# Performance work log

Hardware: AMD Instinct MI355X
Metric: run time of the kernel (lower is better)

The kernel has to match this reference:

```python
import jax, jax.numpy as jnp
import numpy as np

NH, DH, DHR = 16, 128, 64  # heads, head dim, decoupled rope dim
ROPE_BASE = 10000.0

def _rope(x):
    # x: (B, L, H, Dr) with Dr even; interleaved-pair RoPE (torchtune style)
    B, L, H, Dr = x.shape
    pos = jnp.arange(L, dtype=jnp.float32)
    inv_freq = 1.0 / (ROPE_BASE ** (jnp.arange(0, Dr, 2, dtype=jnp.float32) / Dr))
    ang = pos[:, None] * inv_freq[None, :]          # (L, Dr/2)
    cos = jnp.cos(ang)[None, :, None, :].astype(x.dtype)
    sin = jnp.sin(ang)[None, :, None, :].astype(x.dtype)
    x1, x2 = x[..., 0::2], x[..., 1::2]
    out = jnp.stack([x1 * cos - x2 * sin, x1 * sin + x2 * cos], axis=-1)
    return out.reshape(B, L, H, Dr)

def setup_inputs() -> dict:
    key = jax.random.key(0)
    ks = jax.random.split(key, 9)
    s = 0.02
    return {
        'x':     jax.random.normal(ks[0], (2, 2048, 2048), jnp.float32),
        'W_DKV': jax.random.normal(ks[1], (2048, 682), jnp.float32) * s,
        'W_UK':  jax.random.normal(ks[2], (682, 2048), jnp.float32) * s,
        'W_UV':  jax.random.normal(ks[3], (682, 2048), jnp.float32) * s,
        'W_KR':  jax.random.normal(ks[4], (2048, 64), jnp.float32) * s,
        'W_DQ':  jax.random.normal(ks[5], (2048, 682), jnp.float32) * s,
        'W_UQ':  jax.random.normal(ks[6], (682, 2048), jnp.float32) * s,
        'W_QR':  jax.random.normal(ks[7], (682, 1024), jnp.float32) * s,
        'W_O':   jax.random.normal(ks[8], (2048, 2048), jnp.float32) * s,
    }

def reference(x, W_DKV, W_UK, W_UV, W_KR, W_DQ, W_UQ, W_QR, W_O):
    B, L, D = x.shape
    # --- KV path ---
    c_KV = x @ W_DKV                                   # (B, L, dc)
    k_C = (c_KV @ W_UK).reshape(B, L, NH, DH)          # content keys
    k_R = _rope((x @ W_KR).reshape(B, L, 1, DHR))      # shared rope key head
    k_R = jnp.broadcast_to(k_R, (B, L, NH, DHR))
    k = jnp.concatenate([k_C, k_R], axis=-1)           # (B, L, NH, DH+DHR)
    v = (c_KV @ W_UV).reshape(B, L, NH, DH)
    # --- Q path ---
    c_Q = x @ W_DQ                                     # (B, L, dc')
    q_C = (c_Q @ W_UQ).reshape(B, L, NH, DH)
    q_R = _rope((c_Q @ W_QR).reshape(B, L, NH, DHR))
    q = jnp.concatenate([q_C, q_R], axis=-1)           # (B, L, NH, DH+DHR)
    # --- attention (causal) ---
    scale = 1.0 / jnp.sqrt(jnp.float32(DH + DHR))
    scores = jnp.einsum('blhd,bmhd->bhlm', q, k) * scale
    causal = jnp.tril(jnp.ones((L, L), dtype=bool))
    scores = jnp.where(causal[None, None], scores, jnp.finfo(scores.dtype).min)
    attn = jax.nn.softmax(scores, axis=-1)
    o = jnp.einsum('bhlm,bmhd->blhd', attn, v).reshape(B, L, NH * DH)
    return o @ W_O
```

## Files before the change

### kernel.cpp

```cpp
#include <hip/hip_runtime.h>
#include <stdint.h>

typedef __attribute__((ext_vector_type(8))) __bf16 bf16x8;
typedef __attribute__((ext_vector_type(4))) float f32x4;

#define DEVI static __device__ __forceinline__

DEVI uint16_t f2b(float f) {
  uint32_t u = __float_as_uint(f);
  u += 0x7FFFu + ((u >> 16) & 1u);
  return (uint16_t)(u >> 16);
}
DEVI float b2f(uint16_t b) { return __uint_as_float(((uint32_t)b) << 16); }

DEVI void gl_lds16(const void* g, void* l) {
  __builtin_amdgcn_global_load_lds((const __attribute__((address_space(1))) void*)g,
                                   (__attribute__((address_space(3))) void*)l, 16, 0, 0);
}

DEVI f32x4 mfma16(bf16x8 a, bf16x8 b, f32x4 c) {
  return __builtin_amdgcn_mfma_f32_16x16x32_bf16(a, b, c, 0, 0, 0);
}

#define BARX asm volatile("s_barrier" ::: "memory")
#define WLG0 asm volatile("s_waitcnt lgkmcnt(0)" ::: "memory")
#define WV4 asm volatile("s_waitcnt vmcnt(4)" ::: "memory")
#define PRIO1 __builtin_amdgcn_s_setprio(1)
#define PRIO0 __builtin_amdgcn_s_setprio(0)

static constexpr size_t OFF_XB = 0;
static constexpr size_t OFF_WD = 8388608;
static constexpr size_t OFF_WUKV = OFF_WD + 3670016;
static constexpr size_t OFF_WUQR = OFF_WUKV + 3145728;
static constexpr size_t OFF_WO = OFF_WUQR + 2359296;
static constexpr size_t OFF_CD = OFF_WO + 4194304;
static constexpr size_t OFF_CUKV = OFF_CD + 7340032;
static constexpr size_t OFF_CUQR = OFF_CUKV + 16777216;
static constexpr size_t OFF_VT = OFF_CUQR + 12582912;

__global__ void pre_kernel(const float* __restrict__ x, const float* __restrict__ Wdkv,
                           const float* __restrict__ Wuk, const float* __restrict__ Wuv,
                           const float* __restrict__ Wkr, const float* __restrict__ Wdq,
                           const float* __restrict__ Wuq, const float* __restrict__ Wqr,
                           const float* __restrict__ Wo, uint16_t* __restrict__ ws) {
  const int bid = blockIdx.x;
  const int t = threadIdx.x;
  if (bid >= 3264) {
    int id = (bid - 3264) * 256 + t;
    float4 v = ((const float4*)x)[id];
    uint16_t o[4] = {f2b(v.x), f2b(v.y), f2b(v.z), f2b(v.w)};
    *(uint64_t*)&ws[OFF_XB + (size_t)id * 4] = *(uint64_t*)o;
    return;
  }
  const float* W;
  uint16_t* Wt;
  int Kw, Nw, Kp, nx, rb;
  if (bid < 384) {
    W = Wdkv; Wt = ws + OFF_WD; Kw = 2048; Nw = 682; Kp = 2048; nx = 12; rb = bid;
  } else if (bid < 768) {
    W = Wdq; Wt = ws + OFF_WD + (size_t)768 * 2048; Kw = 2048; Nw = 682; Kp = 2048; nx = 12; rb = bid - 384;
  } else if (bid < 896) {
    W = Wkr; Wt = ws + OFF_WD + (size_t)1536 * 2048; Kw = 2048; Nw = 64; Kp = 2048; nx = 4; rb = bid - 768;
  } else if (bid < 1280) {
    W = Wuk; Wt = ws + OFF_WUKV; Kw = 682; Nw = 2048; Kp = 768; nx = 32; rb = bid - 896;
  } else if (bid < 1664) {
    W = Wuv; Wt = ws + OFF_WUKV + (size_t)2048 * 768; Kw = 682; Nw = 2048; Kp = 768; nx = 32; rb = bid - 1280;
  } else if (bid < 2048) {
    W = Wuq; Wt = ws + OFF_WUQR; Kw = 682; Nw = 2048; Kp = 768; nx = 32; rb = bid - 1664;
  } else if (bid < 2240) {
    W = Wqr; Wt = ws + OFF_WUQR + (size_t)2048 * 768; Kw = 682; Nw = 1024; Kp = 768; nx = 16; rb = bid - 2048;
  } else {
    W = Wo; Wt = ws + OFF_WO; Kw = 2048; Nw = 2048; Kp = 2048; nx = 32; rb = bid - 2240;
  }
  const int n0 = (rb % nx) * 64, k0 = (rb / nx) * 64;
  __shared__ uint16_t T[64][72];
#pragma unroll
  for (int p = 0; p < 2; ++p) {
    int r = p * 32 + (t >> 3);
    int c0 = (t & 7) * 8;
    int gr = k0 + r;
#pragma unroll
    for (int e = 0; e < 8; ++e) {
      int gc = n0 + c0 + e;
      float v = (gr < Kw && gc < Nw) ? W[(size_t)gr * Nw + gc] : 0.f;
      T[c0 + e][r] = f2b(v);
    }
  }
  __syncthreads();
#pragma unroll
  for (int p = 0; p < 2; ++p) {
    int dr = p * 32 + (t >> 3);
    int mc = (t & 7) * 8;
    uint16_t tmp[8];
#pragma unroll
    for (int e = 0; e < 8; ++e) tmp[e] = T[dr][mc + e];
    *(uint64_t*)&Wt[(size_t)(n0 + dr) * Kp + k0 + mc] = ((uint64_t*)tmp)[0];
    *(uint64_t*)&Wt[(size_t)(n0 + dr) * Kp + k0 + mc + 4] = ((uint64_t*)tmp)[1];
  }
}

template <int BM, bool F32OUT>
__global__ __launch_bounds__(512, 2) void gemm8(const uint16_t* __restrict__ A, int lda,
                                                const uint16_t* __restrict__ Bt,
                                                void* __restrict__ Cv, int ldc, int K) {
  constexpr int MF = BM / 32;
  constexpr int MH = MF / 2;
  constexpr int AL = BM / 128;
  constexpr int ABYTES = BM * 128;
  __shared__ char lds[2 * BM * 128 + 2 * 256 * 128];
  char* const LB = lds + 2 * ABYTES;
  const int tid = threadIdx.x;
  const int lane = tid & 63;
  const int lr = lane & 15, lgb = (lane >> 4) * 16;
  const int wid = tid >> 6;
  const int g = wid >> 2;
  const int wc = (wid & 3) * 64;
  const int rA0 = g * (BM / 2) + lr;
  const int rB0 = wc + lr;
  const size_t row0 = (size_t)blockIdx.y * BM, col0 = (size_t)blockIdx.x * 256;
  const char* Agb = (const char*)(A + row0 * lda);
  const char* Btb = (const char*)(Bt + col0 * K);
  const size_t ldab = (size_t)lda * 2;
  const size_t ldbb = (size_t)K * 2;
  const int nk = K >> 6;
  const int ni = nk >> 1;

  f32x4 acc[MF][4] = {};
  bf16x8 aF[MH][2], bF[4][2];

  auto stageA = [&](int kt, int buf, int hf) {
#pragma unroll
    for (int j = 0; j < AL; ++j) {
      int c = j * 512 + tid;
      int cl = c ^ (((c >> 5) & 1) << 1);
      int row = hf * (BM / 2) + (cl >> 3);
      gl_lds16(Agb + (size_t)row * ldab + (size_t)kt * 128 + (cl & 7) * 16,
               lds + buf * ABYTES + hf * (ABYTES / 2) + (j * 512 + (tid & 0x1C0)) * 16);
    }
  };
  auto stageB = [&](int kt, int buf, int hf) {
#pragma unroll
    for (int j = 0; j < 2; ++j) {
      int c = j * 512 + tid;
      int cl = c ^ (((c >> 5) & 1) << 1);
      int row = hf * 128 + (cl >> 3);
      gl_lds16(Btb + (size_t)row * ldbb + (size_t)kt * 128 + (cl & 7) * 16,
               LB + buf * 32768 + hf * 16384 + (j * 512 + (tid & 0x1C0)) * 16);
    }
  };
  auto ldAm = [&](int buf, int mb) {
#pragma unroll
    for (int m = 0; m < MH; ++m) {
      int r = rA0 + (mb + m) * 16;
      int ro = r * 128;
      int sw = ((r >> 2) & 1) << 5;
#pragma unroll
      for (int kk = 0; kk < 2; ++kk)
        aF[m][kk] = *(const bf16x8*)(lds + buf * ABYTES + ((ro + kk * 64 + lgb) ^ sw));
    }
  };
  auto ldBn = [&](int buf, int nb) {
#pragma unroll
    for (int n = 0; n < 2; ++n) {
      int r = rB0 + (nb + n) * 16;
      int ro = r * 128;
      int sw = ((r >> 2) & 1) << 5;
#pragma unroll
      for (int kk = 0; kk < 2; ++kk)
        bF[nb + n][kk] = *(const bf16x8*)(LB + buf * 32768 + ((ro + kk * 64 + lgb) ^ sw));
    }
  };
  auto mmac = [&](int mb, int nb) {
#pragma unroll
    for (int m = 0; m < MH; ++m)
#pragma unroll
      for (int n = 0; n < 2; ++n)
#pragma unroll
        for (int kk = 0; kk < 2; ++kk)
          acc[mb + m][nb + n] = mfma16(aF[m][kk], bF[nb + n][kk], acc[mb + m][nb + n]);
  };

  stageA(0, 0, 0); stageA(0, 0, 1); stageB(0, 0, 0); stageB(0, 0, 1);
  stageB(1, 1, 0); stageB(1, 1, 1);
  WV4; BARX;

  for (int i = 0; i < ni; ++i) {
    const int t1 = 2 * i + 1;
    const int tn = (2 * i + 2 < nk) ? 2 * i + 2 : nk - 1;
    const int tn1 = (2 * i + 3 < nk) ? 2 * i + 3 : nk - 1;
    ldAm(0, 0); ldBn(0, 0); stageA(t1, 1, 0);
    BARX; WLG0; PRIO1; mmac(0, 0); PRIO0; BARX;
    ldBn(0, 2); stageA(t1, 1, 1);
    BARX; WLG0; PRIO1; mmac(0, 2); PRIO0; BARX;
    ldAm(0, MH); stageB(tn, 0, 0);
    BARX; WLG0; PRIO1; mmac(MH, 0); PRIO0; BARX;
    stageB(tn, 0, 1);
    BARX; PRIO1; mmac(MH, 2); PRIO0; WV4; BARX;
    ldAm(1, 0); ldBn(1, 0); stageA(tn, 0, 0);
    BARX; WLG0; PRIO1; mmac(0, 0); PRIO0; BARX;
    ldBn(1, 2); stageA(tn, 0, 1);
    BARX; WLG0; PRIO1; mmac(0, 2); PRIO0; BARX;
    ldAm(1, MH); stageB(tn1, 1, 0);
    BARX; WLG0; PRIO1; mmac(MH, 0); PRIO0; BARX;
    stageB(tn1, 1, 1);
    BARX; PRIO1; mmac(MH, 2); PRIO0; WV4; BARX;
  }
  asm volatile("s_waitcnt vmcnt(0)" ::: "memory");

#pragma unroll
  for (int m = 0; m < MF; ++m)
#pragma unroll
    for (int n = 0; n < 4; ++n)
#pragma unroll
      for (int j = 0; j < 4; ++j) {
        size_t row = row0 + g * (BM / 2) + m * 16 + (lane >> 4) * 4 + j;
        size_t col = col0 + wc + n * 16 + lr;
        if (F32OUT)
          ((float*)Cv)[row * ldc + col] = acc[m][n][j];
        else
          ((uint16_t*)Cv)[row * ldc + col] = f2b(acc[m][n][j]);
      }
}

__global__ void misc_kernel(uint16_t* __restrict__ cd, uint16_t* __restrict__ cuqr,
                            const uint16_t* __restrict__ cukv, uint16_t* __restrict__ vt) {
  const int bid = blockIdx.x;
  const int t = threadIdx.x;
  if (bid < 512) {
    int id = bid * 256 + t;
    int row = id >> 5, i = id & 31;
    int pos = row & 2047;
    float invf = exp2f(-13.287712379549449f * (float)i / 32.f);
    float ang = (float)pos * invf;
    float s, c;
    sincosf(ang, &s, &c);
    size_t base = (size_t)row * 1792 + 1536 + 2 * i;
    float x1 = b2f(cd[base]), x2 = b2f(cd[base + 1]);
    cd[base] = f2b(x1 * c - x2 * s);
    cd[base + 1] = f2b(x1 * s + x2 * c);
    return;
  }
  if (bid < 8704) {
    int id = (bid - 512) * 256 + t;
    int row = id >> 9;
    int rem = id & 511;
    int h = rem >> 5, i = rem & 31;
    int pos = row & 2047;
    float invf = exp2f(-13.287712379549449f * (float)i / 32.f);
    float ang = (float)pos * invf;
    float s, c;
    sincosf(ang, &s, &c);
    size_t base = (size_t)row * 3072 + 2048 + h * 64 + 2 * i;
    float x1 = b2f(cuqr[base]), x2 = b2f(cuqr[base + 1]);
    cuqr[base] = f2b(x1 * c - x2 * s);
    cuqr[base + 1] = f2b(x1 * s + x2 * c);
    return;
  }
  const int idx = bid - 8704;
  const int mt = idx & 31, dt = (idx >> 5) & 1, bh = idx >> 6;
  const int b = bh >> 4, h = bh & 15;
  const int m0 = mt * 64, d0 = dt * 64;
  __shared__ uint16_t T[64][72];
#pragma unroll
  for (int p = 0; p < 2; ++p) {
    int r = p * 32 + (t >> 3), c8 = (t & 7) * 8;
    const uint16_t* s = &cukv[((size_t)(b * 2048 + m0 + r)) * 4096 + 2048 + h * 128 + d0 + c8];
    uint16_t tmp[8];
    ((uint64_t*)tmp)[0] = ((const uint64_t*)s)[0];
    ((uint64_t*)tmp)[1] = ((const uint64_t*)s)[1];
#pragma unroll
    for (int e = 0; e < 8; ++e) T[c8 + e][r] = tmp[e];
  }
  __syncthreads();
#pragma unroll
  for (int p = 0; p < 2; ++p) {
    int dr = p * 32 + (t >> 3), mc = (t & 7) * 8;
    uint16_t tmp[8];
#pragma unroll
    for (int e = 0; e < 8; ++e) tmp[e] = T[dr][mc + e];
    uint16_t* dstp = &vt[((size_t)(bh * 128 + d0 + dr)) * 2048 + m0 + mc];
    ((uint64_t*)dstp)[0] = ((uint64_t*)tmp)[0];
    ((uint64_t*)dstp)[1] = ((uint64_t*)tmp)[1];
  }
}

__global__ __launch_bounds__(512, 2) void attn_kernel(const uint16_t* __restrict__ cuqr,
                                                      const uint16_t* __restrict__ cukv,
                                                      const uint16_t* __restrict__ cd,
                                                      const uint16_t* __restrict__ vt,
                                                      uint16_t* __restrict__ obuf) {
  __shared__ uint16_t Ks[2][64 * 192];
  __shared__ uint16_t Vs[2][128 * 64];
  __shared__ uint16_t Ps[8 * 16 * 64];
  const int tid = threadIdx.x;
  const int wid = tid >> 6, lane = tid & 63;
  const int lr = lane & 15, lg = lane >> 4;
  const int bid = blockIdx.x;
  const int wg = (bid & 7) * 32 + (bid >> 3);
  const int pairi = wg & 7;
  const int bh = wg >> 3;
  const int b = bh >> 4, h = bh & 15;
  const float sc2 = 0.07216878364870323f * 1.4426950408889634f;

  const char* Kcb = (const char*)cukv + (size_t)b * 2048 * 8192 + h * 256;
  const char* Krb = (const char*)cd + (size_t)b * 2048 * 3584 + 3072;
  const char* Vb = (const char*)vt + (size_t)bh * 524288;
  char* const Ks0 = (char*)Ks[0];
  char* const Vs0 = (char*)Vs[0];
  char* PwB = (char*)(Ps + wid * 1024);

  const char* kbase[3];
  size_t kstep[3];
  int klds[3];
#pragma unroll
  for (int i = 0; i < 3; ++i) {
    int c = i * 512 + tid;
    int r = c / 24, c16 = c % 24;
    klds[i] = r * 384 + ((c16 * 16) ^ ((r & 7) << 4));
    if (c16 < 16) {
      kbase[i] = Kcb + (size_t)r * 8192 + c16 * 16;
      kstep[i] = (size_t)64 * 8192;
    } else {
      kbase[i] = Krb + (size_t)r * 3584 + (c16 - 16) * 16;
      kstep[i] = (size_t)64 * 3584;
    }
  }
  const char* vbase[2];
  int vlds[2];
#pragma unroll
  for (int i = 0; i < 2; ++i) {
    int c = i * 512 + tid;
    int d = c >> 3, c16 = c & 7;
    vlds[i] = d * 128 + ((c16 * 16) ^ ((d & 7) << 4));
    vbase[i] = Vb + (size_t)d * 4096 + c16 * 16;
  }

  for (int ph = 0; ph < 2; ++ph) {
    const int qt = ph ? (15 - pairi) : pairi;
    const int q0 = qt * 128;
    const int nt = 2 * (qt + 1);
    const int qrow = q0 + wid * 16 + lr;
    bf16x8 qf[6];
    {
      const char* Qcp = (const char*)cuqr + (size_t)(b * 2048 + qrow) * 6144 + h * 256 + lg * 16;
      const char* Qrp =
          (const char*)cuqr + (size_t)(b * 2048 + qrow) * 6144 + 4096 + h * 128 + lg * 16;
#pragma unroll
      for (int kb = 0; kb < 4; ++kb) qf[kb] = *(const bf16x8*)(Qcp + kb * 64);
#pragma unroll
      for (int kb = 0; kb < 2; ++kb) qf[4 + kb] = *(const bf16x8*)(Qrp + kb * 64);
    }
    f32x4 o[8] = {};
    float mrun[4], lrun[4];
#pragma unroll
    for (int j = 0; j < 4; ++j) { mrun[j] = -INFINITY; lrun[j] = 0.f; }

    const char* kp[3];
    const char* vp[2];
    bf16x8 kreg[3], vreg[2];
#pragma unroll
    for (int i = 0; i < 3; ++i) kp[i] = kbase[i];
#pragma unroll
    for (int i = 0; i < 2; ++i) vp[i] = vbase[i];
#pragma unroll
    for (int i = 0; i < 3; ++i) { kreg[i] = *(const bf16x8*)kp[i]; kp[i] += kstep[i]; }
#pragma unroll
    for (int i = 0; i < 2; ++i) { vreg[i] = *(const bf16x8*)vp[i]; vp[i] += 128; }
#pragma unroll
    for (int i = 0; i < 3; ++i) *(bf16x8*)(Ks0 + klds[i]) = kreg[i];
#pragma unroll
    for (int i = 0; i < 2; ++i) *(bf16x8*)(Vs0 + vlds[i]) = vreg[i];
    __syncthreads();

    for (int t = 0; t < nt; ++t) {
      const bool more = (t + 1 < nt);
      if (more) {
#pragma unroll
        for (int i = 0; i < 3; ++i) { kreg[i] = *(const bf16x8*)kp[i]; kp[i] += kstep[i]; }
#pragma unroll
        for (int i = 0; i < 2; ++i) { vreg[i] = *(const bf16x8*)vp[i]; vp[i] += 128; }
      }
      const int cb = t & 1;
      const char* KsB = Ks0 + cb * 24576;
      const char* VsB = Vs0 + cb * 16384;
      if (t * 64 <= q0 + wid * 16 + 15) {
        f32x4 s[4] = {};
        __builtin_amdgcn_s_setprio(1);
#pragma unroll
        for (int n = 0; n < 4; ++n) {
          int r = n * 16 + lr;
          const char* kptr = KsB + r * 384;
          int sw = (r & 7) << 4;
#pragma unroll
          for (int kb = 0; kb < 6; ++kb)
            s[n] = mfma16(qf[kb], *(const bf16x8*)(kptr + ((kb * 64 + lg * 16) ^ sw)), s[n]);
        }
        __builtin_amdgcn_s_setprio(0);
        if (t * 64 + 63 > q0 + wid * 16) {
#pragma unroll
          for (int n = 0; n < 4; ++n)
#pragma unroll
            for (int j = 0; j < 4; ++j)
              if (t * 64 + n * 16 + lr > q0 + wid * 16 + lg * 4 + j) s[n][j] = -INFINITY;
        }
        float pm[4];
#pragma unroll
        for (int j = 0; j < 4; ++j) {
          float v = fmaxf(fmaxf(s[0][j], s[1][j]), fmaxf(s[2][j], s[3][j]));
          v = fmaxf(v, __shfl_xor(v, 1));
          v = fmaxf(v, __shfl_xor(v, 2));
          v = fmaxf(v, __shfl_xor(v, 4));
          v = fmaxf(v, __shfl_xor(v, 8));
          pm[j] = v;
        }
        bool exceed = false;
#pragma unroll
        for (int j = 0; j < 4; ++j) exceed |= (pm[j] > mrun[j] + 76.8f);
        if (__any(exceed)) {
          float alpha[4];
#pragma unroll
          for (int j = 0; j < 4; ++j) {
            float mn = fmaxf(mrun[j], pm[j]);
            alpha[j] = exp2f((mrun[j] - mn) * sc2);
            mrun[j] = mn;
            lrun[j] *= alpha[j];
          }
#pragma unroll
          for (int n2 = 0; n2 < 8; ++n2)
#pragma unroll
            for (int j = 0; j < 4; ++j) o[n2][j] *= alpha[j];
        }
        float rs[4] = {0.f, 0.f, 0.f, 0.f};
#pragma unroll
        for (int n = 0; n < 4; ++n)
#pragma unroll
          for (int j = 0; j < 4; ++j) {
            float p = exp2f((s[n][j] - mrun[j]) * sc2);
            rs[j] += p;
            int row = lg * 4 + j;
            *(uint16_t*)(PwB + row * 128 + ((((n * 16 + lr)) * 2) ^ ((row & 7) << 4))) = f2b(p);
          }
#pragma unroll
        for (int j = 0; j < 4; ++j) lrun[j] += rs[j];
        __builtin_amdgcn_s_setprio(1);
#pragma unroll
        for (int kb2 = 0; kb2 < 2; ++kb2) {
          bf16x8 pa = *(const bf16x8*)(PwB + lr * 128 + ((kb2 * 64 + lg * 16) ^ ((lr & 7) << 4)));
#pragma unroll
          for (int n2 = 0; n2 < 8; ++n2) {
            int vr = n2 * 16 + lr;
            o[n2] = mfma16(
                pa, *(const bf16x8*)(VsB + vr * 128 + ((kb2 * 64 + lg * 16) ^ ((vr & 7) << 4))),
                o[n2]);
          }
        }
        __builtin_amdgcn_s_setprio(0);
      }
      if (more) {
        char* KsN = Ks0 + (cb ^ 1) * 24576;
        char* VsN = Vs0 + (cb ^ 1) * 16384;
#pragma unroll
        for (int i = 0; i < 3; ++i) *(bf16x8*)(KsN + klds[i]) = kreg[i];
#pragma unroll
        for (int i = 0; i < 2; ++i) *(bf16x8*)(VsN + vlds[i]) = vreg[i];
      }
      __syncthreads();
    }
#pragma unroll
    for (int j = 0; j < 4; ++j) {
      float v = lrun[j];
      v += __shfl_xor(v, 1);
      v += __shfl_xor(v, 2);
      v += __shfl_xor(v, 4);
      v += __shfl_xor(v, 8);
      lrun[j] = v;
    }
    float inv[4];
#pragma unroll
    for (int j = 0; j < 4; ++j) inv[j] = 1.f / lrun[j];
#pragma unroll
    for (int n2 = 0; n2 < 8; ++n2)
#pragma unroll
      for (int j = 0; j < 4; ++j) {
        size_t row = (size_t)b * 2048 + q0 + wid * 16 + lg * 4 + j;
        size_t col = (size_t)h * 128 + n2 * 16 + lr;
        obuf[row * 2048 + col] = f2b(o[n2][j] * inv[j]);
      }
  }
}

extern "C" void kernel_launch(void* const* d_in, const int* in_sizes, int n_in,
                              void* d_out, int out_size, void* d_ws, size_t ws_size,
                              hipStream_t stream) {
  (void)in_sizes; (void)n_in; (void)out_size; (void)ws_size;
  const float* x = (const float*)d_in[0];
  const float* Wdkv = (const float*)d_in[1];
  const float* Wuk = (const float*)d_in[2];
  const float* Wuv = (const float*)d_in[3];
  const float* Wkr = (const float*)d_in[4];
  const float* Wdq = (const float*)d_in[5];
  const float* Wuq = (const float*)d_in[6];
  const float* Wqr = (const float*)d_in[7];
  const float* Wo = (const float*)d_in[8];
  uint16_t* ws = (uint16_t*)d_ws;

  uint16_t* xb = ws + OFF_XB;
  uint16_t* obuf = ws + OFF_XB;
  uint16_t* wd = ws + OFF_WD;
  uint16_t* wukv = ws + OFF_WUKV;
  uint16_t* wuqr = ws + OFF_WUQR;
  uint16_t* wo = ws + OFF_WO;
  uint16_t* cd = ws + OFF_CD;
  uint16_t* cukv = ws + OFF_CUKV;
  uint16_t* cuqr = ws + OFF_CUQR;
  uint16_t* vtb = ws + OFF_VT;

  pre_kernel<<<11456, 256, 0, stream>>>(x, Wdkv, Wuk, Wuv, Wkr, Wdq, Wuq, Wqr, Wo, ws);
  gemm8<128, false><<<dim3(7, 32), 512, 0, stream>>>(xb, 2048, wd, cd, 1792, 2048);
  gemm8<256, false><<<dim3(16, 16), 512, 0, stream>>>(cd, 1792, wukv, cukv, 4096, 768);
  gemm8<256, false><<<dim3(12, 16), 512, 0, stream>>>(cd + 768, 1792, wuqr, cuqr, 3072, 768);
  misc_kernel<<<10752, 256, 0, stream>>>(cd, cuqr, cukv, vtb);
  attn_kernel<<<256, 512, 0, stream>>>(cuqr, cukv, cd, vtb, obuf);
  gemm8<128, true><<<dim3(8, 32), 512, 0, stream>>>(obuf, 2048, wo, d_out, 2048, 2048);
}
```

Baseline: 265.3 us.

## Add pipelined 128x256 GEMM kernel for down-projection and output projection

Adds a new gemm4p kernel that double-buffers A and B tiles in LDS. Loads are staggered so global-to-LDS copies of the next k-tiles overlap with MFMA work on the current ones, with priority bumps around the MFMA phases. It replaces gemm8<128> for the x@W_D and o@W_O GEMMs to hide memory latency. The cost is higher LDS use (96KB per block) and tighter coupling of barriers to the K-tile count, which assumes nk is even.

```diff
diff --git a/kernel.cpp b/kernel.cpp
--- a/kernel.cpp
+++ b/kernel.cpp
@@ -222,6 +222,115 @@
       }
 }
 
+template <bool F32OUT>
+__global__ __launch_bounds__(512, 2) void gemm4p(const uint16_t* __restrict__ A, int lda,
+                                                 const uint16_t* __restrict__ Bt,
+                                                 void* __restrict__ Cv, int ldc, int K) {
+  constexpr int ABYTES = 128 * 128;
+  __shared__ char lds[2 * ABYTES + 2 * 32768];
+  char* const LB = lds + 2 * ABYTES;
+  const int tid = threadIdx.x;
+  const int lane = tid & 63;
+  const int lr = lane & 15, lgb = (lane >> 4) * 16;
+  const int wid = tid >> 6;
+  const int g = wid >> 2;
+  const int wc = (wid & 3) * 64;
+  const int rA0 = g * 64 + lr;
+  const int rB0 = wc + lr;
+  const size_t row0 = (size_t)blockIdx.y * 128, col0 = (size_t)blockIdx.x * 256;
+  const char* Agb = (const char*)(A + row0 * lda);
+  const char* Btb = (const char*)(Bt + col0 * K);
+  const size_t ldab = (size_t)lda * 2;
+  const size_t ldbb = (size_t)K * 2;
+  const int nk = K >> 6;
+  const int ni = nk >> 1;
+
+  f32x4 acc[4][4] = {};
+  bf16x8 aF[2][2], bF[4][2];
+
+  auto stageA = [&](int kt, int buf) {
+#pragma unroll
+    for (int j = 0; j < 2; ++j) {
+      int c = j * 512 + tid;
+      int cl = c ^ (((c >> 5) & 1) << 1);
+      gl_lds16(Agb + (size_t)(cl >> 3) * ldab + (size_t)kt * 128 + (cl & 7) * 16,
+               lds + buf * ABYTES + (j * 512 + (tid & 0x1C0)) * 16);
+    }
+  };
+  auto stageBfull = [&](int kt, int buf) {
+#pragma unroll
+    for (int j = 0; j < 4; ++j) {
+      int c = j * 512 + tid;
+      int cl = c ^ (((c >> 5) & 1) << 1);
+      gl_lds16(Btb + (size_t)(cl >> 3) * ldbb + (size_t)kt * 128 + (cl & 7) * 16,
+               LB + buf * 32768 + (j * 512 + (tid & 0x1C0)) * 16);
+    }
+  };
+  auto ldAm = [&](int buf, int mb) {
+#pragma unroll
+    for (int m = 0; m < 2; ++m) {
+      int r = rA0 + (mb + m) * 16;
+      int ro = r * 128;
+      int sw = ((r >> 2) & 1) << 5;
+#pragma unroll
+      for (int kk = 0; kk < 2; ++kk)
+        aF[m][kk] = *(const bf16x8*)(lds + buf * ABYTES + ((ro + kk * 64 + lgb) ^ sw));
+    }
+  };
+  auto ldBn4 = [&](int buf) {
+#pragma unroll
+    for (int n = 0; n < 4; ++n) {
+      int r = rB0 + n * 16;
+      int ro = r * 128;
+      int sw = ((r >> 2) & 1) << 5;
+#pragma unroll
+      for (int kk = 0; kk < 2; ++kk)
+        bF[n][kk] = *(const bf16x8*)(LB + buf * 32768 + ((ro + kk * 64 + lgb) ^ sw));
+    }
+  };
+  auto mmac16 = [&](int mb) {
+#pragma unroll
+    for (int m = 0; m < 2; ++m)
+#pragma unroll
+      for (int n = 0; n < 4; ++n)
+#pragma unroll
+        for (int kk = 0; kk < 2; ++kk)
+          acc[mb + m][n] = mfma16(aF[m][kk], bF[n][kk], acc[mb + m][n]);
+  };
+
+  stageA(0, 0); stageBfull(0, 0); stageBfull(1, 1);
+  WV4; BARX;
+
+  for (int i = 0; i < ni; ++i) {
+    const int t1 = 2 * i + 1;
+    const int t2 = (2 * i + 2 < nk) ? 2 * i + 2 : nk - 1;
+    const int t3 = (2 * i + 3 < nk) ? 2 * i + 3 : nk - 1;
+    ldAm(0, 0); ldBn4(0); stageA(t1, 1);
+    BARX; WLG0; PRIO1; mmac16(0); PRIO0; BARX;
+    ldAm(0, 2); stageBfull(t2, 0);
+    BARX; WLG0; PRIO1; mmac16(2); PRIO0; WV4; BARX;
+    ldAm(1, 0); ldBn4(1); stageA(t2, 0);
+    BARX; WLG0; PRIO1; mmac16(0); PRIO0; BARX;
+    ldAm(1, 2); stageBfull(t3, 1);
+    BARX; WLG0; PRIO1; mmac16(2); PRIO0; WV4; BARX;
+  }
+  asm volatile("s_waitcnt vmcnt(0)" ::: "memory");
+
+#pragma unroll
+  for (int m = 0; m < 4; ++m)
+#pragma unroll
+    for (int n = 0; n < 4; ++n)
+#pragma unroll
+      for (int j = 0; j < 4; ++j) {
+        size_t row = row0 + g * 64 + m * 16 + (lane >> 4) * 4 + j;
+        size_t col = col0 + wc + n * 16 + lr;
+        if (F32OUT)
+          ((float*)Cv)[row * ldc + col] = acc[m][n][j];
+        else
+          ((uint16_t*)Cv)[row * ldc + col] = f2b(acc[m][n][j]);
+      }
+}
+
 __global__ void misc_kernel(uint16_t* __restrict__ cd, uint16_t* __restrict__ cuqr,
                             const uint16_t* __restrict__ cukv, uint16_t* __restrict__ vt) {
   const int bid = blockIdx.x;
@@ -516,10 +625,10 @@
   uint16_t* vtb = ws + OFF_VT;
 
   pre_kernel<<<11456, 256, 0, stream>>>(x, Wdkv, Wuk, Wuv, Wkr, Wdq, Wuq, Wqr, Wo, ws);
-  gemm8<128, false><<<dim3(7, 32), 512, 0, stream>>>(xb, 2048, wd, cd, 1792, 2048);
+  gemm4p<false><<<dim3(7, 32), 512, 0, stream>>>(xb, 2048, wd, cd, 1792, 2048);
   gemm8<256, false><<<dim3(16, 16), 512, 0, stream>>>(cd, 1792, wukv, cukv, 4096, 768);
   gemm8<256, false><<<dim3(12, 16), 512, 0, stream>>>(cd + 768, 1792, wuqr, cuqr, 3072, 768);
   misc_kernel<<<10752, 256, 0, stream>>>(cd, cuqr, cukv, vtb);
   attn_kernel<<<256, 512, 0, stream>>>(cuqr, cukv, cd, vtb, obuf);
-  gemm8<128, true><<<dim3(8, 32), 512, 0, stream>>>(obuf, 2048, wo, d_out, 2048, 2048);
-}
+  gemm4p<true><<<dim3(8, 32), 512, 0, stream>>>(obuf, 2048, wo, d_out, 2048, 2048);
+}
```

New measurement: 267.0 us. About the same (+0.6%).

## Give each attention wave 32 query rows to reuse K/V fragments across two MFMAs

Applied to the files above, without the earlier changes.

The attention block is cut from 8 waves of 16 query rows to 4 waves of 32 query rows each. Every K and V fragment read from LDS now feeds two MFMAs, which halves LDS read traffic per unit of compute. Each thread also loads twice as many K/V chunks into the shared tiles. In exchange, register pressure roughly doubles (accumulators, Q fragments, softmax state), launch bounds drop to 256 threads with one block, and there are fewer waves per CU to hide latency.

```diff
diff --git a/kernel.cpp b/kernel.cpp
--- a/kernel.cpp
+++ b/kernel.cpp
@@ -284,14 +284,14 @@
   }
 }
 
-__global__ __launch_bounds__(512, 2) void attn_kernel(const uint16_t* __restrict__ cuqr,
+__global__ __launch_bounds__(256, 1) void attn_kernel(const uint16_t* __restrict__ cuqr,
                                                       const uint16_t* __restrict__ cukv,
                                                       const uint16_t* __restrict__ cd,
                                                       const uint16_t* __restrict__ vt,
                                                       uint16_t* __restrict__ obuf) {
   __shared__ uint16_t Ks[2][64 * 192];
   __shared__ uint16_t Vs[2][128 * 64];
-  __shared__ uint16_t Ps[8 * 16 * 64];
+  __shared__ uint16_t Ps[4 * 32 * 64];
   const int tid = threadIdx.x;
   const int wid = tid >> 6, lane = tid & 63;
   const int lr = lane & 15, lg = lane >> 4;
@@ -307,14 +307,14 @@
   const char* Vb = (const char*)vt + (size_t)bh * 524288;
   char* const Ks0 = (char*)Ks[0];
   char* const Vs0 = (char*)Vs[0];
-  char* PwB = (char*)(Ps + wid * 1024);
-
-  const char* kbase[3];
-  size_t kstep[3];
-  int klds[3];
-#pragma unroll
-  for (int i = 0; i < 3; ++i) {
-    int c = i * 512 + tid;
+  char* PwB = (char*)(Ps + wid * 2048);
+
+  const char* kbase[6];
+  size_t kstep[6];
+  int klds[6];
+#pragma unroll
+  for (int i = 0; i < 6; ++i) {
+    int c = i * 256 + tid;
     int r = c / 24, c16 = c % 24;
     klds[i] = r * 384 + ((c16 * 16) ^ ((r & 7) << 4));
     if (c16 < 16) {
@@ -325,11 +325,11 @@
       kstep[i] = (size_t)64 * 3584;
     }
   }
-  const char* vbase[2];
-  int vlds[2];
-#pragma unroll
-  for (int i = 0; i < 2; ++i) {
-    int c = i * 512 + tid;
+  const char* vbase[4];
+  int vlds[4];
+#pragma unroll
+  for (int i = 0; i < 4; ++i) {
+    int c = i * 256 + tid;
     int d = c >> 3, c16 = c & 7;
     vlds[i] = d * 128 + ((c16 * 16) ^ ((d & 7) << 4));
     vbase[i] = Vb + (size_t)d * 4096 + c16 * 16;
@@ -339,52 +339,56 @@
     const int qt = ph ? (15 - pairi) : pairi;
     const int q0 = qt * 128;
     const int nt = 2 * (qt + 1);
-    const int qrow = q0 + wid * 16 + lr;
-    bf16x8 qf[6];
-    {
+    const int qw = q0 + wid * 32;
+    bf16x8 qf[2][6];
+#pragma unroll
+    for (int m = 0; m < 2; ++m) {
+      const int qrow = qw + m * 16 + lr;
       const char* Qcp = (const char*)cuqr + (size_t)(b * 2048 + qrow) * 6144 + h * 256 + lg * 16;
       const char* Qrp =
           (const char*)cuqr + (size_t)(b * 2048 + qrow) * 6144 + 4096 + h * 128 + lg * 16;
 #pragma unroll
-      for (int kb = 0; kb < 4; ++kb) qf[kb] = *(const bf16x8*)(Qcp + kb * 64);
-#pragma unroll
-      for (int kb = 0; kb < 2; ++kb) qf[4 + kb] = *(const bf16x8*)(Qrp + kb * 64);
-    }
-    f32x4 o[8] = {};
-    float mrun[4], lrun[4];
-#pragma unroll
-    for (int j = 0; j < 4; ++j) { mrun[j] = -INFINITY; lrun[j] = 0.f; }
-
-    const char* kp[3];
-    const char* vp[2];
-    bf16x8 kreg[3], vreg[2];
-#pragma unroll
-    for (int i = 0; i < 3; ++i) kp[i] = kbase[i];
-#pragma unroll
-    for (int i = 0; i < 2; ++i) vp[i] = vbase[i];
-#pragma unroll
-    for (int i = 0; i < 3; ++i) { kreg[i] = *(const bf16x8*)kp[i]; kp[i] += kstep[i]; }
-#pragma unroll
-    for (int i = 0; i < 2; ++i) { vreg[i] = *(const bf16x8*)vp[i]; vp[i] += 128; }
-#pragma unroll
-    for (int i = 0; i < 3; ++i) *(bf16x8*)(Ks0 + klds[i]) = kreg[i];
-#pragma unroll
-    for (int i = 0; i < 2; ++i) *(bf16x8*)(Vs0 + vlds[i]) = vreg[i];
+      for (int kb = 0; kb < 4; ++kb) qf[m][kb] = *(const bf16x8*)(Qcp + kb * 64);
+#pragma unroll
+      for (int kb = 0; kb < 2; ++kb) qf[m][4 + kb] = *(const bf16x8*)(Qrp + kb * 64);
+    }
+    f32x4 o[2][8] = {};
+    float mrun[2][4], lrun[2][4];
+#pragma unroll
+    for (int m = 0; m < 2; ++m)
+#pragma unroll
+      for (int j = 0; j < 4; ++j) { mrun[m][j] = -INFINITY; lrun[m][j] = 0.f; }
+
+    const char* kp[6];
+    const char* vp[4];
+    bf16x8 kreg[6], vreg[4];
+#pragma unroll
+    for (int i = 0; i < 6; ++i) kp[i] = kbase[i];
+#pragma unroll
+    for (int i = 0; i < 4; ++i) vp[i] = vbase[i];
+#pragma unroll
+    for (int i = 0; i < 6; ++i) { kreg[i] = *(const bf16x8*)kp[i]; kp[i] += kstep[i]; }
+#pragma unroll
+    for (int i = 0; i < 4; ++i) { vreg[i] = *(const bf16x8*)vp[i]; vp[i] += 128; }
+#pragma unroll
+    for (int i = 0; i < 6; ++i) *(bf16x8*)(Ks0 + klds[i]) = kreg[i];
+#pragma unroll
+    for (int i = 0; i < 4; ++i) *(bf16x8*)(Vs0 + vlds[i]) = vreg[i];
     __syncthreads();
 
     for (int t = 0; t < nt; ++t) {
       const bool more = (t + 1 < nt);
       if (more) {
 #pragma unroll
-        for (int i = 0; i < 3; ++i) { kreg[i] = *(const bf16x8*)kp[i]; kp[i] += kstep[i]; }
-#pragma unroll
-        for (int i = 0; i < 2; ++i) { vreg[i] = *(const bf16x8*)vp[i]; vp[i] += 128; }
+        for (int i = 0; i < 6; ++i) { kreg[i] = *(const bf16x8*)kp[i]; kp[i] += kstep[i]; }
+#pragma unroll
+        for (int i = 0; i < 4; ++i) { vreg[i] = *(const bf16x8*)vp[i]; vp[i] += 128; }
       }
       const int cb = t & 1;
       const char* KsB = Ks0 + cb * 24576;
       const char* VsB = Vs0 + cb * 16384;
-      if (t * 64 <= q0 + wid * 16 + 15) {
-        f32x4 s[4] = {};
+      if (t * 64 <= qw + 31) {
+        f32x4 s[2][4] = {};
         __builtin_amdgcn_s_setprio(1);
 #pragma unroll
         for (int n = 0; n < 4; ++n) {
@@ -392,66 +396,81 @@
           const char* kptr = KsB + r * 384;
           int sw = (r & 7) << 4;
 #pragma unroll
-          for (int kb = 0; kb < 6; ++kb)
-            s[n] = mfma16(qf[kb], *(const bf16x8*)(kptr + ((kb * 64 + lg * 16) ^ sw)), s[n]);
+          for (int kb = 0; kb < 6; ++kb) {
+            bf16x8 kf = *(const bf16x8*)(kptr + ((kb * 64 + lg * 16) ^ sw));
+            s[0][n] = mfma16(qf[0][kb], kf, s[0][n]);
+            s[1][n] = mfma16(qf[1][kb], kf, s[1][n]);
+          }
         }
         __builtin_amdgcn_s_setprio(0);
-        if (t * 64 + 63 > q0 + wid * 16) {
+        if (t * 64 + 63 > qw) {
+#pragma unroll
+          for (int m = 0; m < 2; ++m)
+#pragma unroll
+            for (int n = 0; n < 4; ++n)
+#pragma unroll
+              for (int j = 0; j < 4; ++j)
+                if (t * 64 + n * 16 + lr > qw + m * 16 + lg * 4 + j) s[m][n][j] = -INFINITY;
+        }
+        float pm[2][4];
+#pragma unroll
+        for (int m = 0; m < 2; ++m)
+#pragma unroll
+          for (int j = 0; j < 4; ++j) {
+            float v = fmaxf(fmaxf(s[m][0][j], s[m][1][j]), fmaxf(s[m][2][j], s[m][3][j]));
+            v = fmaxf(v, __shfl_xor(v, 1));
+            v = fmaxf(v, __shfl_xor(v, 2));
+            v = fmaxf(v, __shfl_xor(v, 4));
+            v = fmaxf(v, __shfl_xor(v, 8));
+            pm[m][j] = v;
+          }
+        bool exceed = false;
+#pragma unroll
+        for (int m = 0; m < 2; ++m)
+#pragma unroll
+          for (int j = 0; j < 4; ++j) exceed |= (pm[m][j] > mrun[m][j] + 76.8f);
+        if (__any(exceed)) {
+          float alpha;
+#pragma unroll
+          for (int m = 0; m < 2; ++m)
+#pragma unroll
+            for (int j = 0; j < 4; ++j) {
+              float mn = fmaxf(mrun[m][j], pm[m][j]);
+              alpha = exp2f((mrun[m][j] - mn) * sc2);
+              mrun[m][j] = mn;
+              lrun[m][j] *= alpha;
+#pragma unroll
+              for (int n2 = 0; n2 < 8; ++n2) o[m][n2][j] *= alpha;
+            }
+        }
+#pragma unroll
+        for (int m = 0; m < 2; ++m) {
+          float rs[4] = {0.f, 0.f, 0.f, 0.f};
 #pragma unroll
           for (int n = 0; n < 4; ++n)
 #pragma unroll
-            for (int j = 0; j < 4; ++j)
-              if (t * 64 + n * 16 + lr > q0 + wid * 16 + lg * 4 + j) s[n][j] = -INFINITY;
+            for (int j = 0; j < 4; ++j) {
+              float p = exp2f((s[m][n][j] - mrun[m][j]) * sc2);
+              rs[j] += p;
+              int row = m * 16 + lg * 4 + j;
+              *(uint16_t*)(PwB + row * 128 + ((((n * 16 + lr)) * 2) ^ ((row & 7) << 4))) = f2b(p);
+            }
+#pragma unroll
+          for (int j = 0; j < 4; ++j) lrun[m][j] += rs[j];
         }
-        float pm[4];
-#pragma unroll
-        for (int j = 0; j < 4; ++j) {
-          float v = fmaxf(fmaxf(s[0][j], s[1][j]), fmaxf(s[2][j], s[3][j]));
-          v = fmaxf(v, __shfl_xor(v, 1));
-          v = fmaxf(v, __shfl_xor(v, 2));
-          v = fmaxf(v, __shfl_xor(v, 4));
-          v = fmaxf(v, __shfl_xor(v, 8));
-          pm[j] = v;
-        }
-        bool exceed = false;
-#pragma unroll
-        for (int j = 0; j < 4; ++j) exceed |= (pm[j] > mrun[j] + 76.8f);
-        if (__any(exceed)) {
-          float alpha[4];
-#pragma unroll
-          for (int j = 0; j < 4; ++j) {
-            float mn = fmaxf(mrun[j], pm[j]);
-            alpha[j] = exp2f((mrun[j] - mn) * sc2);
-            mrun[j] = mn;
-            lrun[j] *= alpha[j];
-          }
-#pragma unroll
-          for (int n2 = 0; n2 < 8; ++n2)
-#pragma unroll
-            for (int j = 0; j < 4; ++j) o[n2][j] *= alpha[j];
-        }
-        float rs[4] = {0.f, 0.f, 0.f, 0.f};
-#pragma unroll
-        for (int n = 0; n < 4; ++n)
-#pragma unroll
-          for (int j = 0; j < 4; ++j) {
-            float p = exp2f((s[n][j] - mrun[j]) * sc2);
-            rs[j] += p;
-            int row = lg * 4 + j;
-            *(uint16_t*)(PwB + row * 128 + ((((n * 16 + lr)) * 2) ^ ((row & 7) << 4))) = f2b(p);
-          }
-#pragma unroll
-        for (int j = 0; j < 4; ++j) lrun[j] += rs[j];
         __builtin_amdgcn_s_setprio(1);
 #pragma unroll
         for (int kb2 = 0; kb2 < 2; ++kb2) {
-          bf16x8 pa = *(const bf16x8*)(PwB + lr * 128 + ((kb2 * 64 + lg * 16) ^ ((lr & 7) << 4)));
+          bf16x8 pa0 = *(const bf16x8*)(PwB + lr * 128 + ((kb2 * 64 + lg * 16) ^ ((lr & 7) << 4)));
+          bf16x8 pa1 =
+              *(const bf16x8*)(PwB + (16 + lr) * 128 + ((kb2 * 64 + lg * 16) ^ ((lr & 7) << 4)));
 #pragma unroll
           for (int n2 = 0; n2 < 8; ++n2) {
             int vr = n2 * 16 + lr;
-            o[n2] = mfma16(
-                pa, *(const bf16x8*)(VsB + vr * 128 + ((kb2 * 64 + lg * 16) ^ ((vr & 7) << 4))),
-                o[n2]);
+            bf16x8 vf =
+                *(const bf16x8*)(VsB + vr * 128 + ((kb2 * 64 + lg * 16) ^ ((vr & 7) << 4)));
+            o[0][n2] = mfma16(pa0, vf, o[0][n2]);
+            o[1][n2] = mfma16(pa1, vf, o[1][n2]);
           }
         }
         __builtin_amdgcn_s_setprio(0);
@@ -460,32 +479,37 @@
         char* KsN = Ks0 + (cb ^ 1) * 24576;
         char* VsN = Vs0 + (cb ^ 1) * 16384;
 #pragma unroll
-        for (int i = 0; i < 3; ++i) *(bf16x8*)(KsN + klds[i]) = kreg[i];
-#pragma unroll
-        for (int i = 0; i < 2; ++i) *(bf16x8*)(VsN + vlds[i]) = vreg[i];
+        for (int i = 0; i < 6; ++i) *(bf16x8*)(KsN + klds[i]) = kreg[i];
+#pragma unroll
+        for (int i = 0; i < 4; ++i) *(bf16x8*)(VsN + vlds[i]) = vreg[i];
       }
       __syncthreads();
     }
 #pragma unroll
-    for (int j = 0; j < 4; ++j) {
-      float v = lrun[j];
-      v += __shfl_xor(v, 1);
-      v += __shfl_xor(v, 2);
-      v += __shfl_xor(v, 4);
-      v += __shfl_xor(v, 8);
-      lrun[j] = v;
-    }
-    float inv[4];
-#pragma unroll
-    for (int j = 0; j < 4; ++j) inv[j] = 1.f / lrun[j];
-#pragma unroll
-    for (int n2 = 0; n2 < 8; ++n2)
+    for (int m = 0; m < 2; ++m)
 #pragma unroll
       for (int j = 0; j < 4; ++j) {
-        size_t row = (size_t)b * 2048 + q0 + wid * 16 + lg * 4 + j;
-        size_t col = (size_t)h * 128 + n2 * 16 + lr;
-        obuf[row * 2048 + col] = f2b(o[n2][j] * inv[j]);
+        float v = lrun[m][j];
+        v += __shfl_xor(v, 1);
+        v += __shfl_xor(v, 2);
+        v += __shfl_xor(v, 4);
+        v += __shfl_xor(v, 8);
+        lrun[m][j] = v;
       }
+#pragma unroll
+    for (int m = 0; m < 2; ++m) {
+      float inv[4];
+#pragma unroll
+      for (int j = 0; j < 4; ++j) inv[j] = 1.f / lrun[m][j];
+#pragma unroll
+      for (int n2 = 0; n2 < 8; ++n2)
+#pragma unroll
+        for (int j = 0; j < 4; ++j) {
+          size_t row = (size_t)b * 2048 + qw + m * 16 + lg * 4 + j;
+          size_t col = (size_t)h * 128 + n2 * 16 + lr;
+          obuf[row * 2048 + col] = f2b(o[m][n2][j] * inv[j]);
+        }
+    }
   }
 }
 
@@ -520,6 +544,6 @@
   gemm8<256, false><<<dim3(16, 16), 512, 0, stream>>>(cd, 1792, wukv, cukv, 4096, 768);
   gemm8<256, false><<<dim3(12, 16), 512, 0, stream>>>(cd + 768, 1792, wuqr, cuqr, 3072, 768);
   misc_kernel<<<10752, 256, 0, stream>>>(cd, cuqr, cukv, vtb);
-  attn_kernel<<<256, 512, 0, stream>>>(cuqr, cukv, cd, vtb, obuf);
+  attn_kernel<<<256, 256, 0, stream>>>(cuqr, cukv, cd, vtb, obuf);
   gemm8<128, true><<<dim3(8, 32), 512, 0, stream>>>(obuf, 2048, wo, d_out, 2048, 2048);
 }
```

Result: slower. 326.7 us (+23.1%).
